# Kernel optimization log

Hardware: AMD Instinct MI355X
Metric: run time of the kernel (lower is better)

Reference implementation:

```python
import jax, jax.numpy as jnp
import numpy as np

C = 10  # cluster_num
EMB = 64

def setup_inputs() -> dict:
    key = jax.random.key(0)
    ks = jax.random.split(key, 12)
    B, N, D = 8, 4096, 1024
    n_classes = 1
    data = jax.random.normal(ks[0], (B, N, D), dtype=jnp.float32)
    labels = jax.random.randint(ks[1], (B, N), 0, C, dtype=jnp.int32)
    s = 0.02
    return {
        "data": data,
        "labels": labels,
        # embedding_net: Conv2d(1024,64,1) == linear on feature dim
        "W1": jax.random.normal(ks[2], (EMB, D), dtype=jnp.float32) * s,
        "b1": jnp.zeros((EMB,), dtype=jnp.float32),
        # attention MLP: Linear(64,32) -> tanh -> Linear(32,1)
        "Wa1": jax.random.normal(ks[3], (32, EMB), dtype=jnp.float32) * s,
        "ba1": jnp.zeros((32,), dtype=jnp.float32),
        "Wa2": jax.random.normal(ks[4], (1, 32), dtype=jnp.float32) * s,
        "ba2": jnp.zeros((1,), dtype=jnp.float32),
        # fc6: Linear(64,32) -> ReLU -> (Dropout eval=identity) -> Linear(32,n_classes)
        "Wf1": jax.random.normal(ks[5], (32, EMB), dtype=jnp.float32) * s,
        "bf1": jnp.zeros((32,), dtype=jnp.float32),
        "Wf2": jax.random.normal(ks[6], (n_classes, 32), dtype=jnp.float32) * s,
        "bf2": jnp.zeros((n_classes,), dtype=jnp.float32),
    }

def _masked_softmax(x, mask):
    # faithful to the module's numeric trick
    x_masked = x * mask + (1.0 - 1.0 / (mask + 1e-5))
    x_max = jnp.max(x_masked, axis=1, keepdims=True)
    x_exp = jnp.exp(x - x_max) * mask
    return x_exp / jnp.sum(x_exp, axis=1, keepdims=True)

def reference(data, labels, W1, b1, Wa1, ba1, Wa2, ba2, Wf1, bf1, Wf2, bf2):
    B, N, D = data.shape
    # per-patch 1x1-conv embed + ReLU: [B,N,64]
    e = jax.nn.relu(jnp.einsum('bnd,ed->bne', data, W1) + b1)
    # ragged per-cluster mean (AdaptiveAvgPool over each cluster's patches)
    seg = (labels.astype(jnp.int32) + jnp.arange(B, dtype=jnp.int32)[:, None] * C).reshape(-1)
    sums = jax.ops.segment_sum(e.reshape(B * N, EMB), seg, num_segments=B * C)
    counts = jax.ops.segment_sum(jnp.ones((B * N,), dtype=jnp.float32), seg, num_segments=B * C)
    sums = sums.reshape(B, C, EMB)
    counts = counts.reshape(B, C)
    mask = (counts > 0).astype(jnp.float32)
    h = sums / jnp.maximum(counts, 1.0)[..., None]  # [B,C,64]
    # attention scores over clusters
    a = jnp.einsum('bce,oe->bco', jnp.tanh(jnp.einsum('bce,he->bch', h, Wa1) + ba1), Wa2) + ba2
    A = _masked_softmax(a[..., 0], mask)  # [B,C]
    M = jnp.einsum('bc,bce->be', A, h)    # [B,64]
    # fc6 (dropout is identity at inference)
    logits = jax.nn.relu(M @ Wf1.T + bf1) @ Wf2.T + bf2
    return logits
```

## Files before the change

kernel.cpp:

```cpp
#include <hip/hip_runtime.h>
#include <stdint.h>

#define NC 10
#define EMB 64
#define DD 1024
#define NP 4096
#define NB 8
#define BP 128
#define NBLK (NB * NP / BP)
#define PPB (NP / BP)
#define KCH 128
#define NCHUNK (DD / KCH)
#define WFRAG_U32 65536

typedef __attribute__((ext_vector_type(4))) float f32x4;
typedef __attribute__((ext_vector_type(8))) short short8;

union FragU {
    uint32_t u[4];
    int4     i;
    short8   s;
};

__global__ __launch_bounds__(256) void prep_wfrag(
    const float* __restrict__ W1, uint32_t* __restrict__ wf)
{
    const int tid  = blockIdx.x * 256 + threadIdx.x;
    const int lane = tid & 63;
    const int hl   = (tid >> 6) & 1;
    const int ct   = (tid >> 7) & 3;
    const int kg   = tid >> 9;
    const int e    = ct * 16 + (lane & 15);
    const int k0   = kg * 32 + (lane >> 4) * 8;
    const float* src = W1 + (size_t)e * DD + k0;

    uint32_t out[4];
#pragma unroll
    for (int q = 0; q < 4; ++q) {
        float x0 = src[2 * q], x1 = src[2 * q + 1];
        uint32_t b0 = __float_as_uint(x0), b1 = __float_as_uint(x1);
        uint32_t h0 = (b0 + 0x7fffu + ((b0 >> 16) & 1u)) >> 16;
        uint32_t h1 = (b1 + 0x7fffu + ((b1 >> 16) & 1u)) >> 16;
        if (hl == 0) {
            out[q] = h0 | (h1 << 16);
        } else {
            float r0 = x0 - __uint_as_float(h0 << 16);
            float r1 = x1 - __uint_as_float(h1 << 16);
            uint32_t c0 = __float_as_uint(r0), c1 = __float_as_uint(r1);
            uint32_t l0 = (c0 + 0x7fffu + ((c0 >> 16) & 1u)) >> 16;
            uint32_t l1 = (c1 + 0x7fffu + ((c1 >> 16) & 1u)) >> 16;
            out[q] = l0 | (l1 << 16);
        }
    }
    *(uint4*)(wf + (size_t)tid * 4) = make_uint4(out[0], out[1], out[2], out[3]);
}

__global__ __launch_bounds__(512, 2) void embed_mfma(
    const float* __restrict__ data, const int* __restrict__ labels,
    const uint32_t* __restrict__ wf, const float* __restrict__ b1,
    float* __restrict__ psum, float* __restrict__ pcnt, int use_atomic)
{
    __shared__ uint32_t wl[2][8192];
    __shared__ float csum[NC][EMB];
    __shared__ float ccnt[NC];
    __shared__ int   labs[BP];

    const int t    = threadIdx.x;
    const int lane = t & 63;
    const int w    = t >> 6;
    const int bid  = blockIdx.x;
    const int bag  = bid >> 5;
    const int p0   = (bid & 31) * BP;

    for (int i = t; i < NC * EMB; i += 512) (&csum[0][0])[i] = 0.f;
    if (t < NC) ccnt[t] = 0.f;
    if (t < BP) labs[t] = labels[bag * NP + p0 + t];

    const float* Ap = data + (size_t)(bag * NP + p0 + w * 16 + (lane & 15)) * DD
                    + ((lane >> 4) << 3);
    const uint32_t* Wg = wf + (size_t)t * 16;

    f32x4 acc[4] = {};

    float4 aA[8], aB[8];
    uint4  wreg[4];

#pragma unroll
    for (int ks = 0; ks < 4; ++ks) {
        aA[2 * ks]     = *(const float4*)(Ap + ks * 32);
        aA[2 * ks + 1] = *(const float4*)(Ap + ks * 32 + 4);
    }
#pragma unroll
    for (int q = 0; q < 4; ++q) wreg[q] = *(const uint4*)(Wg + q * 4);
#pragma unroll
    for (int q = 0; q < 4; ++q) *(uint4*)&wl[0][t * 16 + q * 4] = wreg[q];
    __syncthreads();

#define PACK_HI(x0, x1) ((__float_as_uint(x1) & 0xffff0000u) | (__float_as_uint(x0) >> 16))
#define SPLIT_KSTEP(ACUR, ks, ahi, alo)                                          \
    {                                                                            \
        const float4 a0 = ACUR[2 * (ks)], a1 = ACUR[2 * (ks) + 1];               \
        ahi.u[0] = PACK_HI(a0.x, a0.y);                                          \
        ahi.u[1] = PACK_HI(a0.z, a0.w);                                          \
        ahi.u[2] = PACK_HI(a1.x, a1.y);                                          \
        ahi.u[3] = PACK_HI(a1.z, a1.w);                                          \
        float r0 = a0.x - __uint_as_float(__float_as_uint(a0.x) & 0xffff0000u);  \
        float r1 = a0.y - __uint_as_float(__float_as_uint(a0.y) & 0xffff0000u);  \
        float r2 = a0.z - __uint_as_float(__float_as_uint(a0.z) & 0xffff0000u);  \
        float r3 = a0.w - __uint_as_float(__float_as_uint(a0.w) & 0xffff0000u);  \
        float r4 = a1.x - __uint_as_float(__float_as_uint(a1.x) & 0xffff0000u);  \
        float r5 = a1.y - __uint_as_float(__float_as_uint(a1.y) & 0xffff0000u);  \
        float r6 = a1.z - __uint_as_float(__float_as_uint(a1.z) & 0xffff0000u);  \
        float r7 = a1.w - __uint_as_float(__float_as_uint(a1.w) & 0xffff0000u);  \
        alo.u[0] = PACK_HI(r0, r1);                                              \
        alo.u[1] = PACK_HI(r2, r3);                                              \
        alo.u[2] = PACK_HI(r4, r5);                                              \
        alo.u[3] = PACK_HI(r6, r7);                                              \
    }

#define CHUNK_BODY(c, BUF, ACUR, ANEXT)                                          \
    {                                                                            \
        if ((c) + 1 < NCHUNK) {                                                  \
            _Pragma("unroll")                                                    \
            for (int ks = 0; ks < 4; ++ks) {                                     \
                ANEXT[2 * ks]     = *(const float4*)(Ap + ((c) + 1) * KCH + ks * 32);      \
                ANEXT[2 * ks + 1] = *(const float4*)(Ap + ((c) + 1) * KCH + ks * 32 + 4);  \
            }                                                                    \
            _Pragma("unroll")                                                    \
            for (int q = 0; q < 4; ++q)                                          \
                wreg[q] = *(const uint4*)(Wg + ((size_t)((c) + 1)) * 8192 + q * 4);        \
        }                                                                        \
        _Pragma("unroll")                                                        \
        for (int ks = 0; ks < 4; ++ks) {                                         \
            FragU ahi, alo;                                                      \
            SPLIT_KSTEP(ACUR, ks, ahi, alo);                                     \
            _Pragma("unroll")                                                    \
            for (int ct = 0; ct < 4; ++ct) {                                     \
                FragU bhi, blo;                                                  \
                bhi.i = *(const int4*)&wl[BUF][((ks * 4 + ct) * 2 + 0) * 256 + lane * 4];  \
                blo.i = *(const int4*)&wl[BUF][((ks * 4 + ct) * 2 + 1) * 256 + lane * 4];  \
                acc[ct] = __builtin_amdgcn_mfma_f32_16x16x32_bf16(ahi.s, bhi.s, acc[ct], 0, 0, 0); \
                acc[ct] = __builtin_amdgcn_mfma_f32_16x16x32_bf16(ahi.s, blo.s, acc[ct], 0, 0, 0); \
                acc[ct] = __builtin_amdgcn_mfma_f32_16x16x32_bf16(alo.s, bhi.s, acc[ct], 0, 0, 0); \
            }                                                                    \
        }                                                                        \
        if ((c) + 1 < NCHUNK) {                                                  \
            _Pragma("unroll")                                                    \
            for (int q = 0; q < 4; ++q)                                          \
                *(uint4*)&wl[(BUF) ^ 1][t * 16 + q * 4] = wreg[q];               \
        }                                                                        \
        __syncthreads();                                                         \
    }

    CHUNK_BODY(0, 0, aA, aB)
    CHUNK_BODY(1, 1, aB, aA)
    CHUNK_BODY(2, 0, aA, aB)
    CHUNK_BODY(3, 1, aB, aA)
    CHUNK_BODY(4, 0, aA, aB)
    CHUNK_BODY(5, 1, aB, aA)
    CHUNK_BODY(6, 0, aA, aB)
    CHUNK_BODY(7, 1, aB, aA)

    float b1v[4];
#pragma unroll
    for (int ct = 0; ct < 4; ++ct) b1v[ct] = b1[ct * 16 + (lane & 15)];
#pragma unroll
    for (int ct = 0; ct < 4; ++ct) {
#pragma unroll
        for (int r = 0; r < 4; ++r) {
            const int patch = w * 16 + (lane >> 4) * 4 + r;
            float v = fmaxf(acc[ct][r] + b1v[ct], 0.f);
            atomicAdd(&csum[labs[patch]][ct * 16 + (lane & 15)], v);
        }
    }
    if (t < BP) atomicAdd(&ccnt[labs[t]], 1.0f);
    __syncthreads();

    if (use_atomic) {
        for (int i = t; i < NC * EMB; i += 512)
            atomicAdd(&psum[(size_t)bag * NC * EMB + i], (&csum[0][0])[i]);
        if (t < NC) atomicAdd(&pcnt[bag * NC + t], ccnt[t]);
    } else {
        for (int i = t; i < NC * EMB; i += 512)
            psum[(size_t)bid * NC * EMB + i] = (&csum[0][0])[i];
        if (t < NC) pcnt[bid * NC + t] = ccnt[t];
    }
}

__global__ __launch_bounds__(256) void head_kernel(
    const float* __restrict__ psum, const float* __restrict__ pcnt, int npb,
    const float* __restrict__ Wa1, const float* __restrict__ ba1,
    const float* __restrict__ Wa2, const float* __restrict__ ba2,
    const float* __restrict__ Wf1, const float* __restrict__ bf1,
    const float* __restrict__ Wf2, const float* __restrict__ bf2,
    float* __restrict__ out)
{
    __shared__ float h[NC][EMB];
    __shared__ float cnt_s[NC];
    __shared__ float mask[NC];
    __shared__ float att[NC][32];
    __shared__ float a_s[NC];
    __shared__ float A_s[NC];
    __shared__ float M_s[EMB];
    __shared__ float f_s[32];

    const int b = blockIdx.x;
    const int t = threadIdx.x;

    if (t < NC) {
        float s = 0.f;
        for (int pb = 0; pb < npb; ++pb) s += pcnt[(size_t)(b * npb + pb) * NC + t];
        cnt_s[t] = s;
        mask[t]  = s > 0.f ? 1.f : 0.f;
    }
    __syncthreads();
    for (int i = t; i < NC * EMB; i += 256) {
        float s = 0.f;
        for (int pb = 0; pb < npb; ++pb) s += psum[(size_t)(b * npb + pb) * NC * EMB + i];
        (&h[0][0])[i] = s / fmaxf(cnt_s[i >> 6], 1.f);
    }
    __syncthreads();

    for (int task = t; task < NC * 32; task += 256) {
        int c = task >> 5, hh = task & 31;
        float s = ba1[hh];
        for (int e = 0; e < EMB; ++e) s = fmaf(Wa1[hh * EMB + e], h[c][e], s);
        att[c][hh] = tanhf(s);
    }
    __syncthreads();

    if (t < NC) {
        float s = ba2[0];
        for (int hh = 0; hh < 32; ++hh) s = fmaf(Wa2[hh], att[t][hh], s);
        a_s[t] = s;
    }
    __syncthreads();

    if (t == 0) {
        float xmax = -1e30f;
        for (int c = 0; c < NC; ++c) {
            float xm = a_s[c] * mask[c] + (1.0f - 1.0f / (mask[c] + 1e-5f));
            xmax = fmaxf(xmax, xm);
        }
        float ex[NC], ssum = 0.f;
        for (int c = 0; c < NC; ++c) {
            ex[c] = expf(a_s[c] - xmax) * mask[c];
            ssum += ex[c];
        }
        for (int c = 0; c < NC; ++c) A_s[c] = ex[c] / ssum;
    }
    __syncthreads();

    if (t < EMB) {
        float s = 0.f;
        for (int c = 0; c < NC; ++c) s = fmaf(A_s[c], h[c][t], s);
        M_s[t] = s;
    }
    __syncthreads();

    if (t < 32) {
        float s = bf1[t];
        for (int e = 0; e < EMB; ++e) s = fmaf(Wf1[t * EMB + e], M_s[e], s);
        f_s[t] = fmaxf(s, 0.f);
    }
    __syncthreads();

    if (t == 0) {
        float s = bf2[0];
        for (int hh = 0; hh < 32; ++hh) s = fmaf(Wf2[hh], f_s[hh], s);
        out[b] = s;
    }
}

extern "C" void kernel_launch(void* const* d_in, const int* in_sizes, int n_in,
                              void* d_out, int out_size, void* d_ws, size_t ws_size,
                              hipStream_t stream)
{
    const float* data   = (const float*)d_in[0];
    const int*   labels = (const int*)  d_in[1];
    const float* W1     = (const float*)d_in[2];
    const float* b1     = (const float*)d_in[3];
    const float* Wa1    = (const float*)d_in[4];
    const float* ba1    = (const float*)d_in[5];
    const float* Wa2    = (const float*)d_in[6];
    const float* ba2    = (const float*)d_in[7];
    const float* Wf1    = (const float*)d_in[8];
    const float* bf1    = (const float*)d_in[9];
    const float* Wf2    = (const float*)d_in[10];
    const float* bf2    = (const float*)d_in[11];

    uint32_t* wfrag = (uint32_t*)d_ws;
    float* psum = (float*)(wfrag + WFRAG_U32);

    prep_wfrag<<<64, 256, 0, stream>>>(W1, wfrag);

    const size_t need_na = (size_t)WFRAG_U32 * 4 +
                           ((size_t)NBLK * NC * EMB + (size_t)NBLK * NC) * sizeof(float);
    if (ws_size >= need_na) {
        float* pcnt = psum + (size_t)NBLK * NC * EMB;
        embed_mfma<<<NBLK, 512, 0, stream>>>(data, labels, wfrag, b1, psum, pcnt, 0);
        head_kernel<<<NB, 256, 0, stream>>>(psum, pcnt, PPB, Wa1, ba1, Wa2, ba2,
                                            Wf1, bf1, Wf2, bf2, (float*)d_out);
    } else {
        float* pcnt = psum + (size_t)NB * NC * EMB;
        hipMemsetAsync((void*)psum, 0,
                       (size_t)(NB * NC * EMB + NB * NC) * sizeof(float), stream);
        embed_mfma<<<NBLK, 512, 0, stream>>>(data, labels, wfrag, b1, psum, pcnt, 1);
        head_kernel<<<NB, 256, 0, stream>>>(psum, pcnt, 1, Wa1, ba1, Wa2, ba2,
                                            Wf1, bf1, Wf2, bf2, (float*)d_out);
    }
}
```

Before: 262.8 us.

## Read W1 fragments from global memory and split embedding columns across wave pairs

Removes the double-buffered shared-memory staging of the bf16 W1 fragments, along with its per-chunk barriers. Each wave now loads its B fragments straight from global memory, relying on the L1/L2 cache. Blocks grow to 1024 threads, with each pair of waves sharing 16 patches and splitting the 64 output columns in half, so each wave keeps two accumulators instead of four. This cuts register and LDS pressure and the syncs between chunks. In exchange, each data row is now loaded by two waves, and weight loads have higher latency and are no longer prefetched.

```diff
diff --git a/kernel.cpp b/kernel.cpp
--- a/kernel.cpp
+++ b/kernel.cpp
@@ -55,12 +55,11 @@
     *(uint4*)(wf + (size_t)tid * 4) = make_uint4(out[0], out[1], out[2], out[3]);
 }
 
-__global__ __launch_bounds__(512, 2) void embed_mfma(
+__global__ __launch_bounds__(1024, 4) void embed_mfma(
     const float* __restrict__ data, const int* __restrict__ labels,
     const uint32_t* __restrict__ wf, const float* __restrict__ b1,
     float* __restrict__ psum, float* __restrict__ pcnt, int use_atomic)
 {
-    __shared__ uint32_t wl[2][8192];
     __shared__ float csum[NC][EMB];
     __shared__ float ccnt[NC];
     __shared__ int   labs[BP];
@@ -68,33 +67,29 @@
     const int t    = threadIdx.x;
     const int lane = t & 63;
     const int w    = t >> 6;
+    const int pt   = w >> 1;
+    const int ch   = w & 1;
     const int bid  = blockIdx.x;
     const int bag  = bid >> 5;
     const int p0   = (bid & 31) * BP;
 
-    for (int i = t; i < NC * EMB; i += 512) (&csum[0][0])[i] = 0.f;
+    for (int i = t; i < NC * EMB; i += 1024) (&csum[0][0])[i] = 0.f;
     if (t < NC) ccnt[t] = 0.f;
     if (t < BP) labs[t] = labels[bag * NP + p0 + t];
-
-    const float* Ap = data + (size_t)(bag * NP + p0 + w * 16 + (lane & 15)) * DD
+    __syncthreads();
+
+    const float* Ap = data + (size_t)(bag * NP + p0 + pt * 16 + (lane & 15)) * DD
                     + ((lane >> 4) << 3);
-    const uint32_t* Wg = wf + (size_t)t * 16;
-
-    f32x4 acc[4] = {};
-
+    const uint4* Wp = (const uint4*)wf + (size_t)(ch * 256 + lane);
+
+    f32x4 acc[2] = {};
     float4 aA[8], aB[8];
-    uint4  wreg[4];
 
 #pragma unroll
     for (int ks = 0; ks < 4; ++ks) {
         aA[2 * ks]     = *(const float4*)(Ap + ks * 32);
         aA[2 * ks + 1] = *(const float4*)(Ap + ks * 32 + 4);
     }
-#pragma unroll
-    for (int q = 0; q < 4; ++q) wreg[q] = *(const uint4*)(Wg + q * 4);
-#pragma unroll
-    for (int q = 0; q < 4; ++q) *(uint4*)&wl[0][t * 16 + q * 4] = wreg[q];
-    __syncthreads();
 
 #define PACK_HI(x0, x1) ((__float_as_uint(x1) & 0xffff0000u) | (__float_as_uint(x0) >> 16))
 #define SPLIT_KSTEP(ACUR, ks, ahi, alo)                                          \
@@ -118,7 +113,7 @@
         alo.u[3] = PACK_HI(r6, r7);                                              \
     }
 
-#define CHUNK_BODY(c, BUF, ACUR, ANEXT)                                          \
+#define CHUNK(c, ACUR, ANEXT)                                                    \
     {                                                                            \
         if ((c) + 1 < NCHUNK) {                                                  \
             _Pragma("unroll")                                                    \
@@ -126,62 +121,52 @@
                 ANEXT[2 * ks]     = *(const float4*)(Ap + ((c) + 1) * KCH + ks * 32);      \
                 ANEXT[2 * ks + 1] = *(const float4*)(Ap + ((c) + 1) * KCH + ks * 32 + 4);  \
             }                                                                    \
-            _Pragma("unroll")                                                    \
-            for (int q = 0; q < 4; ++q)                                          \
-                wreg[q] = *(const uint4*)(Wg + ((size_t)((c) + 1)) * 8192 + q * 4);        \
         }                                                                        \
         _Pragma("unroll")                                                        \
         for (int ks = 0; ks < 4; ++ks) {                                         \
             FragU ahi, alo;                                                      \
             SPLIT_KSTEP(ACUR, ks, ahi, alo);                                     \
             _Pragma("unroll")                                                    \
-            for (int ct = 0; ct < 4; ++ct) {                                     \
+            for (int ct2 = 0; ct2 < 2; ++ct2) {                                  \
                 FragU bhi, blo;                                                  \
-                bhi.i = *(const int4*)&wl[BUF][((ks * 4 + ct) * 2 + 0) * 256 + lane * 4];  \
-                blo.i = *(const int4*)&wl[BUF][((ks * 4 + ct) * 2 + 1) * 256 + lane * 4];  \
-                acc[ct] = __builtin_amdgcn_mfma_f32_16x16x32_bf16(ahi.s, bhi.s, acc[ct], 0, 0, 0); \
-                acc[ct] = __builtin_amdgcn_mfma_f32_16x16x32_bf16(ahi.s, blo.s, acc[ct], 0, 0, 0); \
-                acc[ct] = __builtin_amdgcn_mfma_f32_16x16x32_bf16(alo.s, bhi.s, acc[ct], 0, 0, 0); \
+                bhi.i = *(const int4*)&Wp[(size_t)(((c) * 4 + ks) * 512 + ct2 * 128)];       \
+                blo.i = *(const int4*)&Wp[(size_t)(((c) * 4 + ks) * 512 + ct2 * 128 + 64)];  \
+                acc[ct2] = __builtin_amdgcn_mfma_f32_16x16x32_bf16(ahi.s, bhi.s, acc[ct2], 0, 0, 0); \
+                acc[ct2] = __builtin_amdgcn_mfma_f32_16x16x32_bf16(ahi.s, blo.s, acc[ct2], 0, 0, 0); \
+                acc[ct2] = __builtin_amdgcn_mfma_f32_16x16x32_bf16(alo.s, bhi.s, acc[ct2], 0, 0, 0); \
             }                                                                    \
         }                                                                        \
-        if ((c) + 1 < NCHUNK) {                                                  \
-            _Pragma("unroll")                                                    \
-            for (int q = 0; q < 4; ++q)                                          \
-                *(uint4*)&wl[(BUF) ^ 1][t * 16 + q * 4] = wreg[q];               \
-        }                                                                        \
-        __syncthreads();                                                         \
-    }
-
-    CHUNK_BODY(0, 0, aA, aB)
-    CHUNK_BODY(1, 1, aB, aA)
-    CHUNK_BODY(2, 0, aA, aB)
-    CHUNK_BODY(3, 1, aB, aA)
-    CHUNK_BODY(4, 0, aA, aB)
-    CHUNK_BODY(5, 1, aB, aA)
-    CHUNK_BODY(6, 0, aA, aB)
-    CHUNK_BODY(7, 1, aB, aA)
-
-    float b1v[4];
-#pragma unroll
-    for (int ct = 0; ct < 4; ++ct) b1v[ct] = b1[ct * 16 + (lane & 15)];
-#pragma unroll
-    for (int ct = 0; ct < 4; ++ct) {
+    }
+
+    CHUNK(0, aA, aB)
+    CHUNK(1, aB, aA)
+    CHUNK(2, aA, aB)
+    CHUNK(3, aB, aA)
+    CHUNK(4, aA, aB)
+    CHUNK(5, aB, aA)
+    CHUNK(6, aA, aB)
+    CHUNK(7, aB, aA)
+
+#pragma unroll
+    for (int ct2 = 0; ct2 < 2; ++ct2) {
+        const int emb = (2 * ch + ct2) * 16 + (lane & 15);
+        const float bb = b1[emb];
 #pragma unroll
         for (int r = 0; r < 4; ++r) {
-            const int patch = w * 16 + (lane >> 4) * 4 + r;
-            float v = fmaxf(acc[ct][r] + b1v[ct], 0.f);
-            atomicAdd(&csum[labs[patch]][ct * 16 + (lane & 15)], v);
+            const int patch = pt * 16 + (lane >> 4) * 4 + r;
+            float v = fmaxf(acc[ct2][r] + bb, 0.f);
+            atomicAdd(&csum[labs[patch]][emb], v);
         }
     }
     if (t < BP) atomicAdd(&ccnt[labs[t]], 1.0f);
     __syncthreads();
 
     if (use_atomic) {
-        for (int i = t; i < NC * EMB; i += 512)
+        for (int i = t; i < NC * EMB; i += 1024)
             atomicAdd(&psum[(size_t)bag * NC * EMB + i], (&csum[0][0])[i]);
         if (t < NC) atomicAdd(&pcnt[bag * NC + t], ccnt[t]);
     } else {
-        for (int i = t; i < NC * EMB; i += 512)
+        for (int i = t; i < NC * EMB; i += 1024)
             psum[(size_t)bid * NC * EMB + i] = (&csum[0][0])[i];
         if (t < NC) pcnt[bid * NC + t] = ccnt[t];
     }
@@ -298,14 +283,14 @@
                            ((size_t)NBLK * NC * EMB + (size_t)NBLK * NC) * sizeof(float);
     if (ws_size >= need_na) {
         float* pcnt = psum + (size_t)NBLK * NC * EMB;
-        embed_mfma<<<NBLK, 512, 0, stream>>>(data, labels, wfrag, b1, psum, pcnt, 0);
+        embed_mfma<<<NBLK, 1024, 0, stream>>>(data, labels, wfrag, b1, psum, pcnt, 0);
         head_kernel<<<NB, 256, 0, stream>>>(psum, pcnt, PPB, Wa1, ba1, Wa2, ba2,
                                             Wf1, bf1, Wf2, bf2, (float*)d_out);
     } else {
         float* pcnt = psum + (size_t)NB * NC * EMB;
         hipMemsetAsync((void*)psum, 0,
                        (size_t)(NB * NC * EMB + NB * NC) * sizeof(float), stream);
-        embed_mfma<<<NBLK, 512, 0, stream>>>(data, labels, wfrag, b1, psum, pcnt, 1);
+        embed_mfma<<<NBLK, 1024, 0, stream>>>(data, labels, wfrag, b1, psum, pcnt, 1);
         head_kernel<<<NB, 256, 0, stream>>>(psum, pcnt, 1, Wa1, ba1, Wa2, ba2,
                                             Wf1, bf1, Wf2, bf2, (float*)d_out);
     }
```

Measured after the change: 276.2 us. +5.1%, slower.
